# Kernel optimization log

Measured on AMD Instinct MI355X. Metric: run time of the kernel, lower is better.

Reference implementation:

```python
import jax, jax.numpy as jnp
import numpy as np

NUM_USERS = 100_000
NUM_ITEMS = 50_000
N = NUM_USERS + NUM_ITEMS
E_DIR = 600_000            # directed user->item interactions
E = 2 * E_DIR              # bidirectional edge list used by LGConv
D = 64                     # embed_dim
F_EDGE = 8                 # edge_mlp_input_dim (edge_attr 7 + edge_weight_init 1)
H_MLP = 32                 # edge_mlp_hidden_dim
NUM_ARTISTS = 20_000
NUM_ALBUMS = 40_000
NUM_LAYERS = 3
AUDIO_SCALE = 0.3
META_SCALE = 0.44


def l2norm(x, eps=1e-12):
    # matches torch F.normalize(p=2, dim=-1)
    n = jnp.linalg.norm(x, axis=-1, keepdims=True)
    return x / jnp.maximum(n, eps)


def setup_inputs() -> dict:
    key = jax.random.key(0)
    ks = jax.random.split(key, 12)
    u = jax.random.randint(ks[0], (E_DIR,), 0, NUM_USERS)
    it = jax.random.randint(ks[1], (E_DIR,), 0, NUM_ITEMS) + NUM_USERS
    # bidirectional edges over the concatenated [user; item] node space
    edge_index = jnp.stack([jnp.concatenate([u, it]), jnp.concatenate([it, u])], axis=0)
    return {
        'user_emb_w': 0.01 * jax.random.normal(ks[2], (NUM_USERS, D), jnp.float32),
        'item_audio_emb': jax.random.normal(ks[3], (NUM_ITEMS, D), jnp.float32),
        'artist_emb_w': jax.random.normal(ks[4], (NUM_ARTISTS, D), jnp.float32) * (6.0 / (NUM_ARTISTS + D)) ** 0.5,
        'album_emb_w': jax.random.normal(ks[5], (NUM_ALBUMS, D), jnp.float32) * (6.0 / (NUM_ALBUMS + D)) ** 0.5,
        'mlp_w1': jax.random.normal(ks[6], (F_EDGE, H_MLP), jnp.float32) * (1.0 / F_EDGE) ** 0.5,
        'mlp_b1': jnp.zeros((H_MLP,), jnp.float32),
        'mlp_w2': jax.random.normal(ks[7], (H_MLP, 1), jnp.float32) * (1.0 / H_MLP) ** 0.5,
        'mlp_b2': jnp.zeros((1,), jnp.float32),
        'edge_features': jax.random.uniform(ks[8], (E, F_EDGE), jnp.float32),
        'edge_index': edge_index,
        'artist_ids': jax.random.randint(ks[9], (NUM_ITEMS,), 0, NUM_ARTISTS),
        'album_ids': jax.random.randint(ks[10], (NUM_ITEMS,), 0, NUM_ALBUMS),
    }


def reference(user_emb_w, item_audio_emb, artist_emb_w, album_emb_w,
              mlp_w1, mlp_b1, mlp_w2, mlp_b2, edge_features,
              edge_index, artist_ids, album_ids):
    # Edge weight MLP: Linear -> ReLU -> Linear -> Sigmoid -> squeeze
    h = jax.nn.relu(edge_features @ mlp_w1 + mlp_b1)
    edge_w = jax.nn.sigmoid(h @ mlp_w2 + mlp_b2)[:, 0]  # [E]

    # Node features
    user = l2norm(user_emb_w)
    meta = artist_emb_w[artist_ids] + album_emb_w[album_ids]
    item = l2norm(item_audio_emb * AUDIO_SCALE + meta * META_SCALE)
    x = jnp.concatenate([user, item], axis=0)  # [N, D]

    row, col = edge_index[0], edge_index[1]

    # gcn_norm (add_self_loops=False): deg over destination column
    deg = jax.ops.segment_sum(edge_w, col, num_segments=N)
    dinv = jnp.where(deg > 0, 1.0 / jnp.sqrt(jnp.where(deg > 0, deg, 1.0)), 0.0)
    norm = dinv[row] * edge_w * dinv[col]  # [E]

    acc = x
    for _ in range(NUM_LAYERS):
        msg = norm[:, None] * x[row]                         # gather [E, D]
        x = jax.ops.segment_sum(msg, col, num_segments=N)    # scatter-add
        acc = acc + x
    x = l2norm(acc / (NUM_LAYERS + 1))

    user_emb = x[:NUM_USERS]
    item_emb = x[NUM_USERS:]
    align_loss = jnp.float32(0.0)
    return user_emb, item_emb, align_loss
```

## Files before the change

### kernel.cpp

```cpp
#include <hip/hip_runtime.h>
#include <math.h>

#define NUM_USERS 100000
#define NUM_ITEMS 50000
#define NN 150000
#define EE 1200000
#define NB 586
#define NNP (NB * 256)
#define G8_BLOCKS 4688

typedef unsigned short ushort_t;
typedef unsigned int uint_t;

__device__ __forceinline__ uint_t pack2(float lo, float hi) {
    uint_t a = __float_as_uint(lo);
    uint_t b = __float_as_uint(hi);
    a = (a + 0x7FFFu + ((a >> 16) & 1u)) >> 16;
    b = (b + 0x7FFFu + ((b >> 16) & 1u)) & 0xFFFF0000u;
    return a | b;
}
__device__ __forceinline__ float lo16(uint_t x) { return __uint_as_float(x << 16); }
__device__ __forceinline__ float hi16(uint_t x) { return __uint_as_float(x & 0xFFFF0000u); }

__global__ void mlp_count_kernel(const float* __restrict__ feats,
                                 const float* __restrict__ w1,
                                 const float* __restrict__ b1,
                                 const float* __restrict__ w2,
                                 const float* __restrict__ b2,
                                 const int* __restrict__ col,
                                 int2* __restrict__ er,
                                 int* __restrict__ counts) {
    __shared__ float sw1t[256];
    __shared__ float2 shb[32];
    __shared__ float sb2s;
    int t = threadIdx.x;
    sw1t[t] = w1[(t & 7) * 32 + (t >> 3)];
    if (t < 32) shb[t] = make_float2(b1[t], w2[t]);
    if (t == 0) sb2s = b2[0];
    __syncthreads();
    int e = blockIdx.x * 256 + t;
    if (e >= EE) return;
    int c = col[e];
    const float4* fp = (const float4*)(feats + (size_t)e * 8);
    float4 fa = fp[0], fb = fp[1];
    float f[8] = {fa.x, fa.y, fa.z, fa.w, fb.x, fb.y, fb.z, fb.w};
    float s = sb2s;
#pragma unroll
    for (int j = 0; j < 32; ++j) {
        float4 wa = *(const float4*)&sw1t[j * 8];
        float4 wb = *(const float4*)&sw1t[j * 8 + 4];
        float2 bw = shb[j];
        float h = bw.x;
        h = fmaf(f[0], wa.x, h);
        h = fmaf(f[1], wa.y, h);
        h = fmaf(f[2], wa.z, h);
        h = fmaf(f[3], wa.w, h);
        h = fmaf(f[4], wb.x, h);
        h = fmaf(f[5], wb.y, h);
        h = fmaf(f[6], wb.z, h);
        h = fmaf(f[7], wb.w, h);
        h = fmaxf(h, 0.f);
        s = fmaf(h, bw.y, s);
    }
    float w = 1.f / (1.f + expf(-s));
    int k = atomicAdd(&counts[c], 1);
    er[e] = make_int2(k, __float_as_int(w));
}

__global__ void scan1_kernel(const int* __restrict__ counts,
                             int* __restrict__ offs,
                             int* __restrict__ partials) {
    int i = blockIdx.x * 256 + threadIdx.x;
    int lane = threadIdx.x & 63;
    int v = counts[i];
    int s = v;
#pragma unroll
    for (int off = 1; off < 64; off <<= 1) {
        int u = __shfl_up(s, off, 64);
        if (lane >= off) s += u;
    }
    __shared__ int wsum[4];
    if (lane == 63) wsum[threadIdx.x >> 6] = s;
    __syncthreads();
    int add = 0;
    for (int w = 0; w < (threadIdx.x >> 6); ++w) add += wsum[w];
    offs[i] = s - v + add;
    if (threadIdx.x == 255) partials[blockIdx.x] = s + add;
}

__global__ void scan23_kernel(int* __restrict__ offs,
                              const int* __restrict__ partials) {
    __shared__ int sp[768];
    __shared__ int wsum[4];
    int t = threadIdx.x;
#pragma unroll
    for (int k = 0; k < 3; ++k) {
        int idx = t + k * 256;
        sp[idx] = (idx < NB) ? partials[idx] : 0;
    }
    __syncthreads();
    int v0 = sp[3 * t], v1 = sp[3 * t + 1], v2 = sp[3 * t + 2];
    int tot = v0 + v1 + v2;
    int lane = t & 63;
    int s = tot;
#pragma unroll
    for (int off = 1; off < 64; off <<= 1) {
        int u = __shfl_up(s, off, 64);
        if (lane >= off) s += u;
    }
    if (lane == 63) wsum[t >> 6] = s;
    __syncthreads();
    int add = 0;
    for (int w = 0; w < (t >> 6); ++w) add += wsum[w];
    int excl = s - tot + add;
    sp[3 * t]     = excl;
    sp[3 * t + 1] = excl + v0;
    sp[3 * t + 2] = excl + v0 + v1;
    __syncthreads();
    int base = sp[blockIdx.x];
    int i = blockIdx.x * 256 + t;
    offs[i] = offs[i] + base;
}

__global__ void fill_kernel(const int2* __restrict__ er,
                            const int* __restrict__ row,
                            const int* __restrict__ col,
                            const int* __restrict__ offs,
                            int2* __restrict__ packed) {
    int e = blockIdx.x * 256 + threadIdx.x;
    if (e >= EE) return;
    int2 p = er[e];
    int slot = offs[col[e]] + p.x;
    packed[slot] = make_int2(row[e], p.y);
}

__device__ __forceinline__ void gather_node8(const ushort_t* __restrict__ zin,
                                             const int2* __restrict__ packed,
                                             int beg, int end, unsigned c,
                                             float4& a0, float4& a1) {
    for (int base = beg; base < end; base += 8) {
        int m = end - base; if (m > 8) m = 8;
        int r = 0; float w = 0.f;
        if ((int)c < m) {
            int2 p = packed[base + (int)c];
            r = p.x; w = __int_as_float(p.y);
        }
        int rj[8]; float wj[8]; uint4 vj[8];
#pragma unroll
        for (int u = 0; u < 8; ++u) {
            int idx = (u < m) ? u : (m - 1);
            rj[u] = __shfl(r, idx, 8);
            wj[u] = __shfl(w, u, 8);
        }
#pragma unroll
        for (int u = 0; u < 8; ++u)
            vj[u] = *(const uint4*)(zin + (size_t)(uint_t)rj[u] * 64u + c * 8u);
#pragma unroll
        for (int u = 0; u < 8; ++u) {
            float ww = wj[u]; uint4 v = vj[u];
            a0.x = fmaf(ww, lo16(v.x), a0.x);
            a0.y = fmaf(ww, hi16(v.x), a0.y);
            a0.z = fmaf(ww, lo16(v.y), a0.z);
            a0.w = fmaf(ww, hi16(v.y), a0.w);
            a1.x = fmaf(ww, lo16(v.z), a1.x);
            a1.y = fmaf(ww, hi16(v.z), a1.y);
            a1.z = fmaf(ww, lo16(v.w), a1.z);
            a1.w = fmaf(ww, hi16(v.w), a1.w);
        }
    }
}

__global__ void dinv_init_kernel(const int2* __restrict__ packed,
                                 const int* __restrict__ offs,
                                 const float* __restrict__ user_w,
                                 const float* __restrict__ audio,
                                 const float* __restrict__ artist_w,
                                 const float* __restrict__ album_w,
                                 const int* __restrict__ artist_ids,
                                 const int* __restrict__ album_ids,
                                 float* __restrict__ dinv,
                                 ushort_t* __restrict__ z0) {
    unsigned t = blockIdx.x * 256u + threadIdx.x;
    unsigned node = t >> 3, c = t & 7u;
    if (node >= NN) return;
    int beg = offs[node], end = offs[node + 1];
    float ds = 0.f;
    for (int k = beg + (int)c; k < end; k += 8) ds += __int_as_float(packed[k].y);
    ds += __shfl_xor(ds, 1, 8);
    ds += __shfl_xor(ds, 2, 8);
    ds += __shfl_xor(ds, 4, 8);
    float d = (ds > 0.f) ? rsqrtf(ds) : 0.f;
    if (c == 0) dinv[node] = d;

    size_t ri = (size_t)node * 64u + c * 8u;
    float v[8];
    if (node < NUM_USERS) {
        float4 x0 = *(const float4*)(user_w + ri);
        float4 x1 = *(const float4*)(user_w + ri + 4);
        v[0]=x0.x; v[1]=x0.y; v[2]=x0.z; v[3]=x0.w;
        v[4]=x1.x; v[5]=x1.y; v[6]=x1.z; v[7]=x1.w;
    } else {
        unsigned j = node - NUM_USERS;
        unsigned aid = (unsigned)artist_ids[j], bid = (unsigned)album_ids[j];
        const float* ap = artist_w + (size_t)aid * 64u + c * 8u;
        const float* bp = album_w  + (size_t)bid * 64u + c * 8u;
        const float* up = audio    + (size_t)j   * 64u + c * 8u;
        float4 A0 = *(const float4*)ap, A1 = *(const float4*)(ap + 4);
        float4 B0 = *(const float4*)bp, B1 = *(const float4*)(bp + 4);
        float4 U0 = *(const float4*)up, U1 = *(const float4*)(up + 4);
        v[0] = fmaf(0.44f, A0.x + B0.x, 0.3f * U0.x);
        v[1] = fmaf(0.44f, A0.y + B0.y, 0.3f * U0.y);
        v[2] = fmaf(0.44f, A0.z + B0.z, 0.3f * U0.z);
        v[3] = fmaf(0.44f, A0.w + B0.w, 0.3f * U0.w);
        v[4] = fmaf(0.44f, A1.x + B1.x, 0.3f * U1.x);
        v[5] = fmaf(0.44f, A1.y + B1.y, 0.3f * U1.y);
        v[6] = fmaf(0.44f, A1.z + B1.z, 0.3f * U1.z);
        v[7] = fmaf(0.44f, A1.w + B1.w, 0.3f * U1.w);
    }
    float s = 0.f;
#pragma unroll
    for (int k = 0; k < 8; ++k) s = fmaf(v[k], v[k], s);
    s += __shfl_xor(s, 1, 8);
    s += __shfl_xor(s, 2, 8);
    s += __shfl_xor(s, 4, 8);
    float rn = rsqrtf(fmaxf(s, 1e-24f));
    float scale = ((d > 0.f) ? d : 1.f) * rn;
    uint4 o;
    o.x = pack2(v[0] * scale, v[1] * scale);
    o.y = pack2(v[2] * scale, v[3] * scale);
    o.z = pack2(v[4] * scale, v[5] * scale);
    o.w = pack2(v[6] * scale, v[7] * scale);
    *(uint4*)(z0 + ri) = o;
}

__global__ void spmm_kernel(const ushort_t* __restrict__ zin,
                            const int2* __restrict__ packed,
                            const int* __restrict__ offs,
                            const float* __restrict__ dinv,
                            ushort_t* __restrict__ zout) {
    unsigned t = blockIdx.x * 256u + threadIdx.x;
    unsigned node = t >> 3, c = t & 7u;
    if (node >= NN) return;
    float4 a0 = make_float4(0,0,0,0), a1 = make_float4(0,0,0,0);
    gather_node8(zin, packed, offs[node], offs[node + 1], c, a0, a1);
    float d = dinv[node], dd = d * d;
    uint4 o;
    o.x = pack2(a0.x * dd, a0.y * dd);
    o.y = pack2(a0.z * dd, a0.w * dd);
    o.z = pack2(a1.x * dd, a1.y * dd);
    o.w = pack2(a1.z * dd, a1.w * dd);
    *(uint4*)(zout + (size_t)node * 64u + c * 8u) = o;
}

__global__ void spmm_final_kernel(const ushort_t* __restrict__ z0,
                                  const ushort_t* __restrict__ z1,
                                  const ushort_t* __restrict__ z2,
                                  const int2* __restrict__ packed,
                                  const int* __restrict__ offs,
                                  const float* __restrict__ dinv,
                                  float* __restrict__ out) {
    unsigned t = blockIdx.x * 256u + threadIdx.x;
    unsigned node = t >> 3, c = t & 7u;
    if (node >= NN) return;
    float4 a0 = make_float4(0,0,0,0), a1 = make_float4(0,0,0,0);
    gather_node8(z2, packed, offs[node], offs[node + 1], c, a0, a1);
    float d = dinv[node], dd = d * d;
    size_t ri = (size_t)node * 64u + c * 8u;
    uint4 p0 = *(const uint4*)(z0 + ri);
    uint4 p1 = *(const uint4*)(z1 + ri);
    uint4 p2 = *(const uint4*)(z2 + ri);
    float v[8];
    v[0] = lo16(p0.x) + lo16(p1.x) + lo16(p2.x) + a0.x * dd;
    v[1] = hi16(p0.x) + hi16(p1.x) + hi16(p2.x) + a0.y * dd;
    v[2] = lo16(p0.y) + lo16(p1.y) + lo16(p2.y) + a0.z * dd;
    v[3] = hi16(p0.y) + hi16(p1.y) + hi16(p2.y) + a0.w * dd;
    v[4] = lo16(p0.z) + lo16(p1.z) + lo16(p2.z) + a1.x * dd;
    v[5] = hi16(p0.z) + hi16(p1.z) + hi16(p2.z) + a1.y * dd;
    v[6] = lo16(p0.w) + lo16(p1.w) + lo16(p2.w) + a1.z * dd;
    v[7] = hi16(p0.w) + hi16(p1.w) + hi16(p2.w) + a1.w * dd;
    float s = 0.f;
#pragma unroll
    for (int k = 0; k < 8; ++k) s = fmaf(v[k], v[k], s);
    s += __shfl_xor(s, 1, 8);
    s += __shfl_xor(s, 2, 8);
    s += __shfl_xor(s, 4, 8);
    float n = fmaxf(sqrtf(s) * 0.25f, 1e-12f);
    float inv = 0.25f / n;
    float4 o0 = make_float4(v[0]*inv, v[1]*inv, v[2]*inv, v[3]*inv);
    float4 o1 = make_float4(v[4]*inv, v[5]*inv, v[6]*inv, v[7]*inv);
    *(float4*)(out + ri)     = o0;
    *(float4*)(out + ri + 4) = o1;
    if (t == 0) out[(size_t)NN * 64u] = 0.f;
}

extern "C" void kernel_launch(void* const* d_in, const int* in_sizes, int n_in,
                              void* d_out, int out_size, void* d_ws, size_t ws_size,
                              hipStream_t stream) {
    const float* user_w     = (const float*)d_in[0];
    const float* audio      = (const float*)d_in[1];
    const float* artist_w   = (const float*)d_in[2];
    const float* album_w    = (const float*)d_in[3];
    const float* w1         = (const float*)d_in[4];
    const float* b1         = (const float*)d_in[5];
    const float* w2         = (const float*)d_in[6];
    const float* b2         = (const float*)d_in[7];
    const float* feats      = (const float*)d_in[8];
    const int*   row        = (const int*)d_in[9];
    const int*   col        = row + EE;
    const int*   artist_ids = (const int*)d_in[10];
    const int*   album_ids  = (const int*)d_in[11];
    float* out = (float*)d_out;

    int*      counts   = (int*)d_ws;
    int*      offs     = counts + NNP;
    int*      partials = offs + NNP + 16;
    int2*     er       = (int2*)(partials + 1024);
    float*    dinv     = (float*)(er + EE);
    int2*     packed   = (int2*)(dinv + NN);
    ushort_t* z0       = (ushort_t*)(packed + EE);
    ushort_t* z1       = z0 + (size_t)NN * 64;
    ushort_t* z2       = z1 + (size_t)NN * 64;

    hipMemsetAsync(counts, 0, NNP * sizeof(int), stream);

    mlp_count_kernel<<<(EE + 255) / 256, 256, 0, stream>>>(feats, w1, b1, w2, b2,
                                                           col, er, counts);
    scan1_kernel<<<NB, 256, 0, stream>>>(counts, offs, partials);
    scan23_kernel<<<NB, 256, 0, stream>>>(offs, partials);
    fill_kernel<<<(EE + 255) / 256, 256, 0, stream>>>(er, row, col, offs, packed);
    dinv_init_kernel<<<G8_BLOCKS, 256, 0, stream>>>(packed, offs,
                                                    user_w, audio, artist_w, album_w,
                                                    artist_ids, album_ids, dinv, z0);
    spmm_kernel<<<G8_BLOCKS, 256, 0, stream>>>(z0, packed, offs, dinv, z1);
    spmm_kernel<<<G8_BLOCKS, 256, 0, stream>>>(z1, packed, offs, dinv, z2);
    spmm_final_kernel<<<G8_BLOCKS, 256, 0, stream>>>(z0, z1, z2, packed, offs,
                                                     dinv, out);
}
```

Baseline: 319.9 us.

## Replace atomic counting sort with two-pass bucketed LDS radix sort for CSR build

The CSR construction previously used per-edge global atomics on destination counts, a two-level scan, and a random scatter into the packed array. It now computes edge weights separately, then does a two-level counting sort. The first level builds per-block histograms over 293 coarse buckets of 512 nodes in LDS and scatters records into a temporary buffer that aliases z1. The second level does a per-bucket LDS count, scan and scatter that writes offs and packed. This removes global atomic contention and uncoalesced scatter, at the cost of more kernel launches and an extra pass through a 16-byte-per-edge temporary buffer.

```diff
diff --git a/kernel.cpp b/kernel.cpp
--- a/kernel.cpp
+++ b/kernel.cpp
@@ -5,9 +5,12 @@
 #define NUM_ITEMS 50000
 #define NN 150000
 #define EE 1200000
-#define NB 586
-#define NNP (NB * 256)
+#define NNP 150016
 #define G8_BLOCKS 4688
+
+#define NBUCKET 293
+#define NB2 256
+#define EPB 4688
 
 typedef unsigned short ushort_t;
 typedef unsigned int uint_t;
@@ -22,14 +25,12 @@
 __device__ __forceinline__ float lo16(uint_t x) { return __uint_as_float(x << 16); }
 __device__ __forceinline__ float hi16(uint_t x) { return __uint_as_float(x & 0xFFFF0000u); }
 
-__global__ void mlp_count_kernel(const float* __restrict__ feats,
-                                 const float* __restrict__ w1,
-                                 const float* __restrict__ b1,
-                                 const float* __restrict__ w2,
-                                 const float* __restrict__ b2,
-                                 const int* __restrict__ col,
-                                 int2* __restrict__ er,
-                                 int* __restrict__ counts) {
+__global__ void mlp_kernel(const float* __restrict__ feats,
+                           const float* __restrict__ w1,
+                           const float* __restrict__ b1,
+                           const float* __restrict__ w2,
+                           const float* __restrict__ b2,
+                           float* __restrict__ wout) {
     __shared__ float sw1t[256];
     __shared__ float2 shb[32];
     __shared__ float sb2s;
@@ -40,7 +41,6 @@
     __syncthreads();
     int e = blockIdx.x * 256 + t;
     if (e >= EE) return;
-    int c = col[e];
     const float4* fp = (const float4*)(feats + (size_t)e * 8);
     float4 fa = fp[0], fb = fp[1];
     float f[8] = {fa.x, fa.y, fa.z, fa.w, fb.x, fb.y, fb.z, fb.w};
@@ -62,17 +62,27 @@
         h = fmaxf(h, 0.f);
         s = fmaf(h, bw.y, s);
     }
-    float w = 1.f / (1.f + expf(-s));
-    int k = atomicAdd(&counts[c], 1);
-    er[e] = make_int2(k, __float_as_int(w));
-}
-
-__global__ void scan1_kernel(const int* __restrict__ counts,
-                             int* __restrict__ offs,
-                             int* __restrict__ partials) {
-    int i = blockIdx.x * 256 + threadIdx.x;
-    int lane = threadIdx.x & 63;
-    int v = counts[i];
+    wout[e] = 1.f / (1.f + expf(-s));
+}
+
+__global__ void hist_kernel(const int* __restrict__ col,
+                            int* __restrict__ hist) {
+    __shared__ int h[NBUCKET];
+    int t = threadIdx.x, B = blockIdx.x;
+    for (int i = t; i < NBUCKET; i += 256) h[i] = 0;
+    __syncthreads();
+    int beg = B * EPB, end = beg + EPB; if (end > EE) end = EE;
+    for (int i = beg + t; i < end; i += 256)
+        atomicAdd(&h[col[i] >> 9], 1);
+    __syncthreads();
+    for (int i = t; i < NBUCKET; i += 256) hist[i * NB2 + B] = h[i];
+}
+
+__global__ void scanb_kernel(int* __restrict__ hist,
+                             int* __restrict__ tot) {
+    int b = blockIdx.x, t = threadIdx.x;
+    int v = hist[b * NB2 + t];
+    int lane = t & 63;
     int s = v;
 #pragma unroll
     for (int off = 1; off < 64; off <<= 1) {
@@ -80,58 +90,92 @@
         if (lane >= off) s += u;
     }
     __shared__ int wsum[4];
-    if (lane == 63) wsum[threadIdx.x >> 6] = s;
+    if (lane == 63) wsum[t >> 6] = s;
     __syncthreads();
     int add = 0;
-    for (int w = 0; w < (threadIdx.x >> 6); ++w) add += wsum[w];
-    offs[i] = s - v + add;
-    if (threadIdx.x == 255) partials[blockIdx.x] = s + add;
-}
-
-__global__ void scan23_kernel(int* __restrict__ offs,
-                              const int* __restrict__ partials) {
-    __shared__ int sp[768];
-    __shared__ int wsum[4];
+    for (int w = 0; w < (t >> 6); ++w) add += wsum[w];
+    hist[b * NB2 + t] = s - v + add;
+    if (t == 255) tot[b] = s + add;
+}
+
+__global__ void scant_kernel(const int* __restrict__ tot,
+                             int* __restrict__ base) {
     int t = threadIdx.x;
-#pragma unroll
-    for (int k = 0; k < 3; ++k) {
-        int idx = t + k * 256;
-        sp[idx] = (idx < NB) ? partials[idx] : 0;
-    }
-    __syncthreads();
-    int v0 = sp[3 * t], v1 = sp[3 * t + 1], v2 = sp[3 * t + 2];
-    int tot = v0 + v1 + v2;
+    int v = (t < NBUCKET) ? tot[t] : 0;
     int lane = t & 63;
-    int s = tot;
+    int s = v;
 #pragma unroll
     for (int off = 1; off < 64; off <<= 1) {
         int u = __shfl_up(s, off, 64);
         if (lane >= off) s += u;
     }
+    __shared__ int wsum[8];
     if (lane == 63) wsum[t >> 6] = s;
     __syncthreads();
     int add = 0;
     for (int w = 0; w < (t >> 6); ++w) add += wsum[w];
-    int excl = s - tot + add;
-    sp[3 * t]     = excl;
-    sp[3 * t + 1] = excl + v0;
-    sp[3 * t + 2] = excl + v0 + v1;
-    __syncthreads();
-    int base = sp[blockIdx.x];
-    int i = blockIdx.x * 256 + t;
-    offs[i] = offs[i] + base;
-}
-
-__global__ void fill_kernel(const int2* __restrict__ er,
-                            const int* __restrict__ row,
-                            const int* __restrict__ col,
-                            const int* __restrict__ offs,
-                            int2* __restrict__ packed) {
-    int e = blockIdx.x * 256 + threadIdx.x;
-    if (e >= EE) return;
-    int2 p = er[e];
-    int slot = offs[col[e]] + p.x;
-    packed[slot] = make_int2(row[e], p.y);
+    if (t < NBUCKET) base[t] = s - v + add;
+    if (t == 511) base[NBUCKET] = s + add;
+}
+
+__global__ void scatter1_kernel(const int* __restrict__ col,
+                                const int* __restrict__ row,
+                                const float* __restrict__ wbuf,
+                                const int* __restrict__ hist,
+                                const int* __restrict__ base,
+                                int4* __restrict__ tmp) {
+    __shared__ int bbase[NBUCKET];
+    __shared__ int cur[NBUCKET];
+    int t = threadIdx.x, B = blockIdx.x;
+    for (int i = t; i < NBUCKET; i += 256) {
+        bbase[i] = base[i] + hist[i * NB2 + B];
+        cur[i] = 0;
+    }
+    __syncthreads();
+    int beg = B * EPB, end = beg + EPB; if (end > EE) end = EE;
+    for (int i = beg + t; i < end; i += 256) {
+        int c = col[i];
+        int b = c >> 9;
+        int r = atomicAdd(&cur[b], 1);
+        tmp[bbase[b] + r] = make_int4(c, row[i], __float_as_int(wbuf[i]), 0);
+    }
+}
+
+__global__ void scatter2_kernel(const int4* __restrict__ tmp,
+                                const int* __restrict__ base,
+                                int* __restrict__ offs,
+                                int2* __restrict__ packed) {
+    __shared__ int sc[512];
+    __shared__ int wsum[8];
+    int b = blockIdx.x, t = threadIdx.x;
+    int beg = base[b], end = base[b + 1];
+    sc[t] = 0;
+    __syncthreads();
+    for (int i = beg + t; i < end; i += 512)
+        atomicAdd(&sc[tmp[i].x & 511], 1);
+    __syncthreads();
+    int v = sc[t];
+    int lane = t & 63;
+    int s = v;
+#pragma unroll
+    for (int off = 1; off < 64; off <<= 1) {
+        int u = __shfl_up(s, off, 64);
+        if (lane >= off) s += u;
+    }
+    if (lane == 63) wsum[t >> 6] = s;
+    __syncthreads();
+    int add = 0;
+    for (int w = 0; w < (t >> 6); ++w) add += wsum[w];
+    int excl = s - v + add;
+    offs[b * 512 + t] = beg + excl;
+    __syncthreads();
+    sc[t] = excl;
+    __syncthreads();
+    for (int i = beg + t; i < end; i += 512) {
+        int4 rec = tmp[i];
+        int r = atomicAdd(&sc[rec.x & 511], 1);
+        packed[beg + r] = make_int2(rec.y, rec.z);
+    }
 }
 
 __device__ __forceinline__ void gather_node8(const ushort_t* __restrict__ zin,
@@ -311,23 +355,24 @@
     const int*   album_ids  = (const int*)d_in[11];
     float* out = (float*)d_out;
 
-    int*      counts   = (int*)d_ws;
-    int*      offs     = counts + NNP;
-    int*      partials = offs + NNP + 16;
-    int2*     er       = (int2*)(partials + 1024);
-    float*    dinv     = (float*)(er + EE);
-    int2*     packed   = (int2*)(dinv + NN);
-    ushort_t* z0       = (ushort_t*)(packed + EE);
-    ushort_t* z1       = z0 + (size_t)NN * 64;
-    ushort_t* z2       = z1 + (size_t)NN * 64;
-
-    hipMemsetAsync(counts, 0, NNP * sizeof(int), stream);
-
-    mlp_count_kernel<<<(EE + 255) / 256, 256, 0, stream>>>(feats, w1, b1, w2, b2,
-                                                           col, er, counts);
-    scan1_kernel<<<NB, 256, 0, stream>>>(counts, offs, partials);
-    scan23_kernel<<<NB, 256, 0, stream>>>(offs, partials);
-    fill_kernel<<<(EE + 255) / 256, 256, 0, stream>>>(er, row, col, offs, packed);
+    int*      hist    = (int*)d_ws;
+    int*      tot     = hist + NBUCKET * NB2;
+    int*      base    = tot + 512;
+    int*      offs    = base + 512;
+    float*    wbuf    = (float*)(offs + NNP + 16);
+    float*    dinv    = wbuf + EE;
+    int2*     packed  = (int2*)(dinv + NN);
+    ushort_t* z0      = (ushort_t*)(packed + EE);
+    ushort_t* z1      = z0 + (size_t)NN * 64;
+    ushort_t* z2      = z1 + (size_t)NN * 64;
+    int4*     tmp     = (int4*)z1;
+
+    mlp_kernel<<<(EE + 255) / 256, 256, 0, stream>>>(feats, w1, b1, w2, b2, wbuf);
+    hist_kernel<<<NB2, 256, 0, stream>>>(col, hist);
+    scanb_kernel<<<NBUCKET, 256, 0, stream>>>(hist, tot);
+    scant_kernel<<<1, 512, 0, stream>>>(tot, base);
+    scatter1_kernel<<<NB2, 256, 0, stream>>>(col, row, wbuf, hist, base, tmp);
+    scatter2_kernel<<<NBUCKET, 512, 0, stream>>>(tmp, base, offs, packed);
     dinv_init_kernel<<<G8_BLOCKS, 256, 0, stream>>>(packed, offs,
                                                     user_w, audio, artist_w, album_w,
                                                     artist_ids, album_ids, dinv, z0);
```

New measurement: 300.3 us. 6.1% less time.
